# Kernel optimization log

Hardware: AMD Instinct MI355X
Metric: run time of the kernel (lower is better)

The kernel has to match this reference:

```python
import jax, jax.numpy as jnp
from jax import lax
import numpy as np

# Static config (see init_kwargs)
D_MODEL = 1024
K = 32          # num_heads
K_Q = 4         # num_query_heads
N_ANCHOR = 4
N_DECAY = K - N_ANCHOR  # 28
M = 8           # num_thetas
KS = 4          # conv kernel size
H = D_MODEL // K  # 32 (expand_factor=1 -> d_inner = d_model)
N_REP = K // K_Q  # 8
DIM_K = D_MODEL
DIM_DECAY = K
DIM_Q = K_Q * H * M * 2  # 2048
TOTAL = DIM_K + DIM_DECAY + DIM_Q  # 3104
B, L = 2, 2048


def setup_inputs() -> dict:
    key = jax.random.key(0)
    ks = jax.random.split(key, 8)
    x = jax.random.normal(ks[0], (B, L, D_MODEL), jnp.float32)
    W_in = jax.random.normal(ks[1], (D_MODEL, TOTAL), jnp.float32) * (D_MODEL ** -0.5)
    # depthwise causal conv kernel: (width, in_per_group=1, channels)
    conv_k = jax.random.normal(ks[2], (KS, 1, DIM_K + DIM_DECAY), jnp.float32) * 0.3
    # theta init (M > 1 branch): linspace(-pi/3, pi/3, M) tiled over (1,1,K,H,M)
    grid = np.linspace(-np.pi / 3, np.pi / 3, M)
    theta = jnp.asarray(np.tile(grid.reshape(1, 1, 1, 1, M), (1, 1, K, H, 1)), jnp.float32)
    decay_slopes = jnp.log(jnp.exp(jnp.asarray(np.geomspace(0.001, 0.1, N_DECAY), jnp.float32)) - 1.0)
    anchor_slopes = jnp.log(jnp.exp(jnp.asarray(np.geomspace(0.01, 0.1, N_ANCHOR), jnp.float32)) - 1.0)
    score_scale = jnp.ones((K,), jnp.float32)
    lim = float(np.sqrt(6.0 / (H + H)))  # glorot uniform
    W_re = jax.random.uniform(ks[3], (H, H), jnp.float32, -lim, lim)
    W_im = jax.random.uniform(ks[4], (H, H), jnp.float32, -lim, lim)
    norm_scale = jnp.ones((2 * H,), jnp.float32)
    W_out = jax.random.normal(ks[5], (D_MODEL, D_MODEL), jnp.float32) * (D_MODEL ** -0.5)
    return dict(x=x, W_in=W_in, conv_k=conv_k, theta=theta, decay_slopes=decay_slopes,
                anchor_slopes=anchor_slopes, score_scale=score_scale, W_re=W_re,
                W_im=W_im, norm_scale=norm_scale, W_out=W_out)


def reference(x, W_in, conv_k, theta, decay_slopes, anchor_slopes, score_scale,
              W_re, W_im, norm_scale, W_out):
    b, l, _ = x.shape
    z = x @ W_in                                    # (b,l,TOTAL)
    z_mem = z[..., :DIM_K + DIM_DECAY]
    q_raw = z[..., DIM_K + DIM_DECAY:]
    # causal depthwise conv over time
    zp = jnp.pad(z_mem, ((0, 0), (KS - 1, 0), (0, 0)))
    z_mem = lax.conv_general_dilated(zp, conv_k, window_strides=(1,), padding='VALID',
                                     dimension_numbers=('NWC', 'WIO', 'NWC'),
                                     feature_group_count=DIM_K + DIM_DECAY)
    k_val = z_mem[..., :DIM_K].reshape(b, l, K, H)
    s_raw = z_mem[..., -K:].reshape(b, l, K, 1)
    q = q_raw.reshape(b, l, K_Q, H, M, 2)
    q_re, q_im = q[..., 0], q[..., 1]
    # ALiBi-like decay / anchor log weights
    pos = jnp.arange(l, dtype=jnp.float32)
    slopes_d = jax.nn.softplus(decay_slopes).reshape(1, 1, N_DECAY, 1)
    dist = jnp.maximum(jnp.float32(l - 1) - pos, 0.0)
    lw_d = -slopes_d * dist[None, :, None, None]        # (1,l,N_DECAY,1)
    slopes_a = jax.nn.softplus(anchor_slopes).reshape(1, 1, N_ANCHOR, 1)
    lw_a = -slopes_a * pos[None, :, None, None]         # (1,l,N_ANCHOR,1)
    log_tw = jnp.concatenate([lw_d, lw_a], axis=2)      # (1,l,K,1)
    log_p = jnp.clip(score_scale[None, None, :, None] * s_raw, -20.0, 20.0)
    p_w = jnp.exp(log_p + log_tw)                       # (b,l,K,1)
    # complex rotary features of keys
    phi = k_val[..., None] * theta                      # (b,l,K,H,M)
    re_k = jnp.cos(phi)
    im_k = jnp.sin(phi)
    # cumulative state
    den = jnp.cumsum(p_w[..., 0], axis=1)               # (b,l,K)
    pwb = p_w[..., None]                                # (b,l,K,1,1)
    num_re = jnp.cumsum(pwb * re_k, axis=1)             # (b,l,K,H,M)
    num_im = jnp.cumsum(pwb * im_k, axis=1)
    inv = lax.rsqrt(jnp.maximum(den, 0.0001))
    inv = (inv * inv)[..., None, None]                  # 1/den, (b,l,K,1,1)
    s_re = (num_re * inv).reshape(b, l, K_Q, N_REP, H, M)
    s_im = (num_im * inv).reshape(b, l, K_Q, N_REP, H, M)
    qr = q_re.reshape(b, l, K_Q, 1, H, M)
    qi = q_im.reshape(b, l, K_Q, 1, H, M)
    out_re = jnp.sum(s_re * qr + s_im * qi, axis=-1).reshape(b, l, K, H)
    out_im = jnp.sum(s_im * qr - s_re * qi, axis=-1).reshape(b, l, K, H)
    # original einsum 'blkh,hh->blkh' uses only the diagonal of W_re / W_im
    y_re = out_re * norm_scale[:H] * jnp.diagonal(W_re)
    y_im = out_im * norm_scale[H:] * jnp.diagonal(W_im)
    y = jax.nn.silu((y_re + y_im).reshape(b, l, DIM_K))
    return y @ W_out
```

## Files before the change

kernel.cpp:

```cpp
#include <hip/hip_runtime.h>
#include <hip/hip_bf16.h>
#include <math.h>

#define D_MODEL   1024
#define K_TOT     32
#define N_DECAY   28
#define M_DIM     8
#define KS        4
#define H_DIM     32
#define DIM_K     1024
#define DIM_MEM   1056
#define DIM_Q     2048
#define TOTAL_DIM 3104
#define NPAD_IN   3328
#define B_SZ      2
#define L_SEQ     2048
#define BL_TOT    4096

#define KG_CNT    4
#define NCHUNK    64
#define CHUNK_L   32

typedef __attribute__((ext_vector_type(8))) __bf16 bf16x8;
typedef __attribute__((ext_vector_type(4))) __bf16 bf16x4;
typedef __attribute__((ext_vector_type(4))) float  f32x4;

__device__ __forceinline__ void gload_lds16(const void* g, void* l) {
    __builtin_amdgcn_global_load_lds(
        (const __attribute__((address_space(1))) void*)g,
        (__attribute__((address_space(3))) void*)l, 16, 0, 0);
}

__global__ __launch_bounds__(512, 2) void gemm_big(const __bf16* __restrict__ A,
                                                   const __bf16* __restrict__ Bt,
                                                   float* __restrict__ C,
                                                   __bf16* __restrict__ Cq,
                                                   int Kdim, int gx) {
    __shared__ __bf16 lds[2][2][256 * 64];

    const int tid  = threadIdx.x;
    const int w    = tid >> 6;
    const int lane = tid & 63;
    const int l15  = lane & 15;
    const int l16  = lane >> 4;
    const int wm   = w >> 2;
    const int wn   = w & 3;

    const int nwg = gridDim.x;
    int lin = blockIdx.x;
    lin = (lin & 7) * (nwg >> 3) + (lin >> 3);
    const int bx = lin % gx, by = lin / gx;
    const int r0 = by * 256, c0 = bx * 256;

    const int srl   = lane >> 3;
    const int sslot = lane & 7;

    f32x4 acc[8][4] = {};
    const int NT = Kdim / 64;

#define STG_A(T, BUF, J)                                                       \
    {                                                                          \
        const int r_  = (J) * 64 + w * 8 + srl;                                \
        const int so_ = sslot ^ (r_ & 7);                                      \
        gload_lds16(A + (size_t)(r0 + r_) * Kdim + (T) * 64 + so_ * 8,         \
                    &lds[BUF][0][((J) * 64 + w * 8) * 64]);                    \
    }
#define STG_B(T, BUF, J)                                                       \
    {                                                                          \
        const int r_  = (J) * 64 + w * 8 + srl;                                \
        const int so_ = sslot ^ (r_ & 7);                                      \
        gload_lds16(Bt + (size_t)(c0 + r_) * Kdim + (T) * 64 + so_ * 8,        \
                    &lds[BUF][1][((J) * 64 + w * 8) * 64]);                    \
    }

#define LOAD_A(AP, MIBASE)                                                     \
    _Pragma("unroll") for (int m2 = 0; m2 < 2; m2++)                           \
        _Pragma("unroll") for (int kk = 0; kk < 2; kk++) {                     \
            const int row_  = wm * 128 + ((MIBASE) + m2) * 16 + l15;           \
            const int slot_ = (kk * 4 + l16) ^ (row_ & 7);                     \
            AP[m2][kk] = *(const bf16x8*)&As_[row_ * 64 + slot_ * 8];          \
        }

#define PHASE(AP, MIBASE)                                                      \
    __builtin_amdgcn_s_barrier();                                              \
    asm volatile("s_waitcnt lgkmcnt(0)" ::: "memory");                         \
    __builtin_amdgcn_sched_barrier(0);                                         \
    __builtin_amdgcn_s_setprio(1);                                             \
    _Pragma("unroll") for (int kk = 0; kk < 2; kk++)                           \
        _Pragma("unroll") for (int m2 = 0; m2 < 2; m2++)                       \
            _Pragma("unroll") for (int ni = 0; ni < 4; ni++)                   \
                acc[(MIBASE) + m2][ni] =                                       \
                    __builtin_amdgcn_mfma_f32_16x16x32_bf16(                   \
                        AP[m2][kk], b[ni][kk], acc[(MIBASE) + m2][ni], 0,0,0); \
    __builtin_amdgcn_s_setprio(0);                                             \
    __builtin_amdgcn_sched_barrier(0);                                         \
    __builtin_amdgcn_s_barrier();

#pragma unroll
    for (int j = 0; j < 4; j++) { STG_A(0, 0, j); STG_B(0, 0, j); }
#pragma unroll
    for (int j = 0; j < 4; j++) { STG_A(1, 1, j); STG_B(1, 1, j); }
    __builtin_amdgcn_sched_barrier(0);
    asm volatile("s_waitcnt vmcnt(8)" ::: "memory");
    __builtin_amdgcn_s_barrier();
    __builtin_amdgcn_sched_barrier(0);

    for (int t = 0; t < NT; ++t) {
        const int cur = t & 1;
        const __bf16* As_ = &lds[cur][0][0];
        const __bf16* Bs_ = &lds[cur][1][0];
        const bool pf = (t + 2 < NT);
        const int tn = t + 2;

        bf16x8 b[4][2], ap[2][2];

#pragma unroll
        for (int ni = 0; ni < 4; ni++)
#pragma unroll
            for (int kk = 0; kk < 2; kk++) {
                const int col  = wn * 64 + ni * 16 + l15;
                const int slot = (kk * 4 + l16) ^ (col & 7);
                b[ni][kk] = *(const bf16x8*)&Bs_[col * 64 + slot * 8];
            }
        LOAD_A(ap, 0);
        PHASE(ap, 0);

        LOAD_A(ap, 2);
        if (pf) { STG_B(tn, cur, 0); STG_B(tn, cur, 1); }
        PHASE(ap, 2);

        LOAD_A(ap, 4);
        if (pf) { STG_B(tn, cur, 2); STG_B(tn, cur, 3);
                  STG_A(tn, cur, 0); STG_A(tn, cur, 2); }
        PHASE(ap, 4);

        LOAD_A(ap, 6);
        PHASE(ap, 6);

        if (pf) { STG_A(tn, cur, 1); STG_A(tn, cur, 3); }
        __builtin_amdgcn_sched_barrier(0);
        if (pf) asm volatile("s_waitcnt vmcnt(8)" ::: "memory");
        else    asm volatile("s_waitcnt vmcnt(0)" ::: "memory");
        __builtin_amdgcn_s_barrier();
        __builtin_amdgcn_sched_barrier(0);
    }
#undef STG_A
#undef STG_B
#undef LOAD_A
#undef PHASE

#pragma unroll
    for (int mi = 0; mi < 8; mi++) {
#pragma unroll
        for (int ni = 0; ni < 4; ni++) {
            const int col = c0 + wn * 64 + ni * 16 + l15;
            const int row = r0 + wm * 128 + mi * 16 + l16 * 4;
            if (col < DIM_MEM) {
#pragma unroll
                for (int q = 0; q < 4; q++)
                    C[(size_t)(row + q) * DIM_MEM + col] = acc[mi][ni][q];
            } else if (col < TOTAL_DIM) {
#pragma unroll
                for (int q = 0; q < 4; q++)
                    Cq[(size_t)(row + q) * DIM_Q + (col - DIM_MEM)] =
                        (__bf16)acc[mi][ni][q];
            }
        }
    }
}

__global__ __launch_bounds__(512, 2) void gemm_mid(const __bf16* __restrict__ A,
                                                   const __bf16* __restrict__ Bt,
                                                   float* __restrict__ C,
                                                   int Ndim, int Kdim, int gx) {
    __shared__ __bf16 lds[2][2][128 * 64];

    const int tid  = threadIdx.x;
    const int w    = tid >> 6;
    const int lane = tid & 63;
    const int l15  = lane & 15;
    const int l16  = lane >> 4;
    const int wm   = w >> 1;
    const int wn   = w & 1;

    const int nwg = gridDim.x;
    int lin = blockIdx.x;
    lin = (lin & 7) * (nwg >> 3) + (lin >> 3);
    const int bx = lin % gx, by = lin / gx;
    const int r0 = by * 128, c0 = bx * 128;

    const int srl   = lane >> 3;
    const int sslot = lane & 7;

    f32x4 acc[2][4] = {};
    const int NT = Kdim / 64;

#define STG4(T, BUF)                                                           \
    _Pragma("unroll") for (int j = 0; j < 2; j++) {                            \
        const int r_  = j * 64 + w * 8 + srl;                                  \
        const int so_ = sslot ^ (r_ & 7);                                      \
        gload_lds16(A + (size_t)(r0 + r_) * Kdim + (T) * 64 + so_ * 8,         \
                    &lds[BUF][0][(j * 64 + w * 8) * 64]);                      \
        gload_lds16(Bt + (size_t)(c0 + r_) * Kdim + (T) * 64 + so_ * 8,        \
                    &lds[BUF][1][(j * 64 + w * 8) * 64]);                      \
    }

    STG4(0, 0);
    STG4(1, 1);
    __builtin_amdgcn_sched_barrier(0);
    asm volatile("s_waitcnt vmcnt(4)" ::: "memory");
    __builtin_amdgcn_s_barrier();
    __builtin_amdgcn_sched_barrier(0);

    for (int t = 0; t < NT; ++t) {
        const int cur = t & 1;
        const __bf16* As_ = &lds[cur][0][0];
        const __bf16* Bs_ = &lds[cur][1][0];
        const bool pf = (t + 2 < NT);

        bf16x8 b[4][2], a[2][2];
#pragma unroll
        for (int ni = 0; ni < 4; ni++)
#pragma unroll
            for (int kk = 0; kk < 2; kk++) {
                const int col  = wn * 64 + ni * 16 + l15;
                const int slot = (kk * 4 + l16) ^ (col & 7);
                b[ni][kk] = *(const bf16x8*)&Bs_[col * 64 + slot * 8];
            }
#pragma unroll
        for (int mi = 0; mi < 2; mi++)
#pragma unroll
            for (int kk = 0; kk < 2; kk++) {
                const int row  = wm * 32 + mi * 16 + l15;
                const int slot = (kk * 4 + l16) ^ (row & 7);
                a[mi][kk] = *(const bf16x8*)&As_[row * 64 + slot * 8];
            }
        asm volatile("s_waitcnt lgkmcnt(0)" ::: "memory");
        __builtin_amdgcn_sched_barrier(0);
        __builtin_amdgcn_s_setprio(1);
#pragma unroll
        for (int kk = 0; kk < 2; kk++)
#pragma unroll
            for (int mi = 0; mi < 2; mi++)
#pragma unroll
                for (int ni = 0; ni < 4; ni++)
                    acc[mi][ni] = __builtin_amdgcn_mfma_f32_16x16x32_bf16(
                        a[mi][kk], b[ni][kk], acc[mi][ni], 0, 0, 0);
        __builtin_amdgcn_s_setprio(0);
        __builtin_amdgcn_sched_barrier(0);
        __builtin_amdgcn_s_barrier();
        if (pf) STG4(t + 2, cur);
        __builtin_amdgcn_sched_barrier(0);
        if (pf) asm volatile("s_waitcnt vmcnt(4)" ::: "memory");
        else    asm volatile("s_waitcnt vmcnt(0)" ::: "memory");
        __builtin_amdgcn_s_barrier();
        __builtin_amdgcn_sched_barrier(0);
    }
#undef STG4

#pragma unroll
    for (int mi = 0; mi < 2; mi++) {
#pragma unroll
        for (int ni = 0; ni < 4; ni++) {
            const int col = c0 + wn * 64 + ni * 16 + l15;
            const int row = r0 + wm * 32 + mi * 16 + l16 * 4;
#pragma unroll
            for (int q = 0; q < 4; q++)
                C[(size_t)(row + q) * Ndim + col] = acc[mi][ni][q];
        }
    }
}

__global__ __launch_bounds__(256) void cast_bf16(const float* __restrict__ in,
                                                 __bf16* __restrict__ out, int n4) {
    const int i = blockIdx.x * blockDim.x + threadIdx.x;
    if (i >= n4) return;
    const float4 v = ((const float4*)in)[i];
    bf16x4 o;
    o.x = (__bf16)v.x; o.y = (__bf16)v.y; o.z = (__bf16)v.z; o.w = (__bf16)v.w;
    ((bf16x4*)out)[i] = o;
}

__global__ __launch_bounds__(256) void transpose_cast(const float* __restrict__ W,
                                                      __bf16* __restrict__ Wt,
                                                      int Kdim, int Ndim, int Npad) {
    __shared__ float tile[32][33];
    const int n0 = blockIdx.x * 32, k0 = blockIdx.y * 32;
    const int tx = threadIdx.x & 31, ty = threadIdx.x >> 5;
#pragma unroll
    for (int i = 0; i < 32; i += 8) {
        float v = 0.f;
        if (n0 + tx < Ndim) v = W[(size_t)(k0 + ty + i) * Ndim + n0 + tx];
        tile[ty + i][tx] = v;
    }
    __syncthreads();
#pragma unroll
    for (int i = 0; i < 32; i += 8) {
        const int n = n0 + ty + i;
        if (n < Npad) Wt[(size_t)n * Kdim + k0 + tx] = (__bf16)tile[tx][ty + i];
    }
}

__global__ __launch_bounds__(256) void conv_pw(const float* __restrict__ z_mem,
                                               const float* __restrict__ conv_k,
                                               const float* __restrict__ score_scale,
                                               const float* __restrict__ decay_slopes,
                                               const float* __restrict__ anchor_slopes,
                                               __bf16* __restrict__ k_val,
                                               float* __restrict__ p_w) {
    const int bl = blockIdx.x;
    const int l = bl & (L_SEQ - 1);
    const int b = bl >> 11;
    const int t = threadIdx.x;

    {
        const int c = 4 * t;
        float4 acc = {0.f, 0.f, 0.f, 0.f};
#pragma unroll
        for (int s = 0; s < KS; s++) {
            const int tl = l - (KS - 1) + s;
            if (tl >= 0) {
                const float4 ck = *(const float4*)&conv_k[s * DIM_MEM + c];
                const float4 zv = *(const float4*)&z_mem[((size_t)b * L_SEQ + tl) * DIM_MEM + c];
                acc.x = fmaf(ck.x, zv.x, acc.x);
                acc.y = fmaf(ck.y, zv.y, acc.y);
                acc.z = fmaf(ck.z, zv.z, acc.z);
                acc.w = fmaf(ck.w, zv.w, acc.w);
            }
        }
        bf16x4 o;
        o.x = (__bf16)acc.x; o.y = (__bf16)acc.y;
        o.z = (__bf16)acc.z; o.w = (__bf16)acc.w;
        *(bf16x4*)&k_val[(size_t)bl * DIM_K + c] = o;
    }

    if (t < 8) {
        const int c = DIM_MEM - K_TOT + 4 * t;
        float acc[4] = {0.f, 0.f, 0.f, 0.f};
#pragma unroll
        for (int s = 0; s < KS; s++) {
            const int tl = l - (KS - 1) + s;
            if (tl >= 0) {
                const float4 ck = *(const float4*)&conv_k[s * DIM_MEM + c];
                const float4 zv = *(const float4*)&z_mem[((size_t)b * L_SEQ + tl) * DIM_MEM + c];
                acc[0] = fmaf(ck.x, zv.x, acc[0]);
                acc[1] = fmaf(ck.y, zv.y, acc[1]);
                acc[2] = fmaf(ck.z, zv.z, acc[2]);
                acc[3] = fmaf(ck.w, zv.w, acc[3]);
            }
        }
#pragma unroll
        for (int j = 0; j < 4; j++) {
            const int k = 4 * t + j;
            const float lp = fminf(fmaxf(score_scale[k] * acc[j], -20.f), 20.f);
            float lt;
            if (k < N_DECAY) {
                const float sd = log1pf(__expf(decay_slopes[k]));
                lt = -sd * (float)(L_SEQ - 1 - l);
            } else {
                const float sa = log1pf(__expf(anchor_slopes[k - N_DECAY]));
                lt = -sa * (float)l;
            }
            p_w[(size_t)bl * K_TOT + k] = __expf(lp + lt);
        }
    }
}

__global__ __launch_bounds__(256) void chunk_sums(const __bf16* __restrict__ k_val,
                                                  const float* __restrict__ p_w,
                                                  const float* __restrict__ theta,
                                                  float* __restrict__ csum,
                                                  float* __restrict__ cden) {
    const int idx = blockIdx.x;
    const int c = idx & (NCHUNK - 1);
    const int bkg = idx / NCHUNK;
    const int kg = bkg & (KG_CNT - 1);
    const int b = bkg / KG_CNT;
    const int t = threadIdx.x;
    const int kl = t >> 5;
    const int h = t & 31;
    const int k = kg * 8 + kl;
    const int bk = b * K_TOT + k;

    const float A0 = theta[(k * H_DIM + h) * M_DIM + 0];
    const float Dt = theta[(k * H_DIM + h) * M_DIM + 1] - A0;

    float nre[M_DIM] = {}, nim[M_DIM] = {};
    float den = 0.f;
    const int l0 = c * CHUNK_L;
#pragma unroll 2
    for (int i = 0; i < CHUNK_L; i++) {
        const size_t bl = (size_t)b * L_SEQ + (l0 + i);
        const float p  = p_w[bl * K_TOT + k];
        const float kv = (float)k_val[bl * DIM_K + k * H_DIM + h];
        float cc = __cosf(kv * A0), ss = __sinf(kv * A0);
        const float cd = __cosf(kv * Dt), sd = __sinf(kv * Dt);
#pragma unroll
        for (int m = 0; m < M_DIM; m++) {
            nre[m] = fmaf(p, cc, nre[m]);
            nim[m] = fmaf(p, ss, nim[m]);
            const float c2 = fmaf(cc, cd, -(ss * sd));
            ss = fmaf(ss, cd, cc * sd);
            cc = c2;
        }
        den += p;
    }

    float* base = &csum[(((size_t)bk * NCHUNK + c) * 256 + h * M_DIM) * 2];
#pragma unroll
    for (int j = 0; j < 4; j++) {
        f32x4 v = { nre[2 * j], nim[2 * j], nre[2 * j + 1], nim[2 * j + 1] };
        ((f32x4*)base)[j] = v;
    }
    if (h == 0) cden[bk * NCHUNK + c] = den;
}

__global__ __launch_bounds__(256) void chunk_prefix(float* __restrict__ csum,
                                                    float* __restrict__ cden) {
    const int bk = blockIdx.x;
    const int t = threadIdx.x;

    if (t < 64) {
        const float orig = cden[bk * NCHUNK + t];
        float v = orig;
#pragma unroll
        for (int d = 1; d < 64; d <<= 1) {
            const float u = __shfl_up(v, d);
            if (t >= d) v += u;
        }
        cden[bk * NCHUNK + t] = v - orig;
    }

    float run_re = 0.f, run_im = 0.f;
    for (int c = 0; c < NCHUNK; c++) {
        float2* p = (float2*)&csum[(((size_t)bk * NCHUNK + c) * 256 + t) * 2];
        const float2 v = *p;
        *p = make_float2(run_re, run_im);
        run_re += v.x;
        run_im += v.y;
    }
}

__global__ __launch_bounds__(256) void scan_out(const __bf16* __restrict__ q_b,
                                                const __bf16* __restrict__ k_val,
                                                const float* __restrict__ p_w,
                                                const float* __restrict__ theta,
                                                const float* __restrict__ csum,
                                                const float* __restrict__ cden,
                                                const float* __restrict__ W_re,
                                                const float* __restrict__ W_im,
                                                const float* __restrict__ norm_scale,
                                                __bf16* __restrict__ y) {
    const int idx = blockIdx.x;
    const int c = idx & (NCHUNK - 1);
    const int bkg = idx / NCHUNK;
    const int kg = bkg & (KG_CNT - 1);
    const int b = bkg / KG_CNT;
    const int t = threadIdx.x;
    const int kl = t >> 5;
    const int h = t & 31;
    const int k = kg * 8 + kl;
    const int bk = b * K_TOT + k;

    const float A0 = theta[(k * H_DIM + h) * M_DIM + 0];
    const float Dt = theta[(k * H_DIM + h) * M_DIM + 1] - A0;

    float nre[M_DIM], nim[M_DIM];
    {
        const float* base = &csum[(((size_t)bk * NCHUNK + c) * 256 + h * M_DIM) * 2];
#pragma unroll
        for (int j = 0; j < 4; j++) {
            const f32x4 v = ((const f32x4*)base)[j];
            nre[2 * j] = v.x; nim[2 * j] = v.y;
            nre[2 * j + 1] = v.z; nim[2 * j + 1] = v.w;
        }
    }
    float den = cden[bk * NCHUNK + c];

    const float wsc_re = norm_scale[h] * W_re[h * H_DIM + h];
    const float wsc_im = norm_scale[H_DIM + h] * W_im[h * H_DIM + h];

    const int l0 = c * CHUNK_L;
    for (int i = 0; i < CHUNK_L; i++) {
        const size_t bl = (size_t)b * L_SEQ + (l0 + i);
        const float p  = p_w[bl * K_TOT + k];
        const float kv = (float)k_val[bl * DIM_K + k * H_DIM + h];

        const __bf16* qp = &q_b[bl * DIM_Q + (size_t)(kg * H_DIM + h) * 16];
        const bf16x8 q0 = *(const bf16x8*)qp;
        const bf16x8 q1 = *(const bf16x8*)(qp + 8);

        float cc = __cosf(kv * A0), ss = __sinf(kv * A0);
        const float cd = __cosf(kv * Dt), sd = __sinf(kv * Dt);

        float ore = 0.f, oim = 0.f;
#pragma unroll
        for (int m = 0; m < M_DIM; m++) {
            nre[m] = fmaf(p, cc, nre[m]);
            nim[m] = fmaf(p, ss, nim[m]);
            const float qr = (m < 4) ? (float)q0[2 * (m & 3)]     : (float)q1[2 * (m & 3)];
            const float qi = (m < 4) ? (float)q0[2 * (m & 3) + 1] : (float)q1[2 * (m & 3) + 1];
            ore = fmaf(nre[m], qr, fmaf(nim[m], qi, ore));
            oim = fmaf(nim[m], qr, fmaf(-nre[m], qi, oim));
            const float c2 = fmaf(cc, cd, -(ss * sd));
            ss = fmaf(ss, cd, cc * sd);
            cc = c2;
        }
        den += p;
        const float inv = __builtin_amdgcn_rcpf(fmaxf(den, 1e-4f));

        const float v = (ore * wsc_re + oim * wsc_im) * inv;
        const float yv = v * __builtin_amdgcn_rcpf(1.0f + __expf(-v));
        y[bl * DIM_K + k * H_DIM + h] = (__bf16)yv;
    }
}

extern "C" void kernel_launch(void* const* d_in, const int* in_sizes, int n_in,
                              void* d_out, int out_size, void* d_ws, size_t ws_size,
                              hipStream_t stream) {
    const float* x            = (const float*)d_in[0];
    const float* W_in         = (const float*)d_in[1];
    const float* conv_k       = (const float*)d_in[2];
    const float* theta        = (const float*)d_in[3];
    const float* decay_slopes = (const float*)d_in[4];
    const float* anchor_slopes= (const float*)d_in[5];
    const float* score_scale  = (const float*)d_in[6];
    const float* W_re         = (const float*)d_in[7];
    const float* W_im         = (const float*)d_in[8];
    const float* norm_scale   = (const float*)d_in[9];
    const float* W_out        = (const float*)d_in[10];
    float* out = (float*)d_out;

    float* ws = (float*)d_ws;
    size_t off = 0;
    float* z_mem  = ws + off; off += (size_t)BL_TOT * DIM_MEM;
    float* p_w    = ws + off; off += (size_t)BL_TOT * K_TOT;
    float* csum   = ws + off; off += (size_t)B_SZ * K_TOT * NCHUNK * 256 * 2;
    float* cden   = ws + off; off += (size_t)B_SZ * K_TOT * NCHUNK;
    __bf16* k_val   = (__bf16*)(ws + off); off += (size_t)BL_TOT * DIM_K / 2;
    __bf16* x_b     = (__bf16*)(ws + off); off += (size_t)BL_TOT * D_MODEL / 2;
    __bf16* W_in_T  = (__bf16*)(ws + off); off += (size_t)NPAD_IN * D_MODEL / 2;
    __bf16* W_out_T = (__bf16*)(ws + off); off += (size_t)D_MODEL * D_MODEL / 2;
    __bf16* y_b     = (__bf16*)(ws + off); off += (size_t)BL_TOT * DIM_K / 2;
    __bf16* q_b     = (__bf16*)(ws + off); off += (size_t)BL_TOT * DIM_Q / 2;

    cast_bf16<<<(BL_TOT * D_MODEL / 4 + 255) / 256, 256, 0, stream>>>(
        x, x_b, BL_TOT * D_MODEL / 4);
    {
        dim3 g(NPAD_IN / 32, D_MODEL / 32);
        transpose_cast<<<g, 256, 0, stream>>>(W_in, W_in_T, D_MODEL, TOTAL_DIM, NPAD_IN);
    }
    {
        dim3 g(D_MODEL / 32, D_MODEL / 32);
        transpose_cast<<<g, 256, 0, stream>>>(W_out, W_out_T, D_MODEL, D_MODEL, D_MODEL);
    }

    gemm_big<<<(NPAD_IN / 256) * (BL_TOT / 256), 512, 0, stream>>>(
        x_b, W_in_T, z_mem, q_b, D_MODEL, NPAD_IN / 256);

    conv_pw<<<BL_TOT, 256, 0, stream>>>(z_mem, conv_k, score_scale, decay_slopes,
                                        anchor_slopes, k_val, p_w);
    chunk_sums<<<B_SZ * KG_CNT * NCHUNK, 256, 0, stream>>>(k_val, p_w, theta, csum, cden);
    chunk_prefix<<<B_SZ * K_TOT, 256, 0, stream>>>(csum, cden);
    scan_out<<<B_SZ * KG_CNT * NCHUNK, 256, 0, stream>>>(q_b, k_val, p_w, theta, csum,
                                                         cden, W_re, W_im, norm_scale, y_b);
    gemm_mid<<<(D_MODEL / 128) * (BL_TOT / 128), 512, 0, stream>>>(
        y_b, W_out_T, out, D_MODEL, D_MODEL, D_MODEL / 128);
}
```

Before: 125.8 us.

## Fuse causal conv and p_w computation into chunk_sums and scan_out

```diff
diff --git a/kernel.cpp b/kernel.cpp
--- a/kernel.cpp
+++ b/kernel.cpp
@@ -301,73 +301,45 @@
     }
 }
 
-__global__ __launch_bounds__(256) void conv_pw(const float* __restrict__ z_mem,
-                                               const float* __restrict__ conv_k,
-                                               const float* __restrict__ score_scale,
-                                               const float* __restrict__ decay_slopes,
-                                               const float* __restrict__ anchor_slopes,
-                                               __bf16* __restrict__ k_val,
-                                               float* __restrict__ p_w) {
-    const int bl = blockIdx.x;
-    const int l = bl & (L_SEQ - 1);
-    const int b = bl >> 11;
-    const int t = threadIdx.x;
-
-    {
-        const int c = 4 * t;
-        float4 acc = {0.f, 0.f, 0.f, 0.f};
-#pragma unroll
-        for (int s = 0; s < KS; s++) {
-            const int tl = l - (KS - 1) + s;
-            if (tl >= 0) {
-                const float4 ck = *(const float4*)&conv_k[s * DIM_MEM + c];
-                const float4 zv = *(const float4*)&z_mem[((size_t)b * L_SEQ + tl) * DIM_MEM + c];
-                acc.x = fmaf(ck.x, zv.x, acc.x);
-                acc.y = fmaf(ck.y, zv.y, acc.y);
-                acc.z = fmaf(ck.z, zv.z, acc.z);
-                acc.w = fmaf(ck.w, zv.w, acc.w);
-            }
-        }
-        bf16x4 o;
-        o.x = (__bf16)acc.x; o.y = (__bf16)acc.y;
-        o.z = (__bf16)acc.z; o.w = (__bf16)acc.w;
-        *(bf16x4*)&k_val[(size_t)bl * DIM_K + c] = o;
-    }
-
-    if (t < 8) {
-        const int c = DIM_MEM - K_TOT + 4 * t;
-        float acc[4] = {0.f, 0.f, 0.f, 0.f};
-#pragma unroll
-        for (int s = 0; s < KS; s++) {
-            const int tl = l - (KS - 1) + s;
-            if (tl >= 0) {
-                const float4 ck = *(const float4*)&conv_k[s * DIM_MEM + c];
-                const float4 zv = *(const float4*)&z_mem[((size_t)b * L_SEQ + tl) * DIM_MEM + c];
-                acc[0] = fmaf(ck.x, zv.x, acc[0]);
-                acc[1] = fmaf(ck.y, zv.y, acc[1]);
-                acc[2] = fmaf(ck.z, zv.z, acc[2]);
-                acc[3] = fmaf(ck.w, zv.w, acc[3]);
-            }
-        }
-#pragma unroll
-        for (int j = 0; j < 4; j++) {
-            const int k = 4 * t + j;
-            const float lp = fminf(fmaxf(score_scale[k] * acc[j], -20.f), 20.f);
-            float lt;
-            if (k < N_DECAY) {
-                const float sd = log1pf(__expf(decay_slopes[k]));
-                lt = -sd * (float)(L_SEQ - 1 - l);
-            } else {
-                const float sa = log1pf(__expf(anchor_slopes[k - N_DECAY]));
-                lt = -sa * (float)l;
-            }
-            p_w[(size_t)bl * K_TOT + k] = __expf(lp + lt);
-        }
-    }
-}
-
-__global__ __launch_bounds__(256) void chunk_sums(const __bf16* __restrict__ k_val,
-                                                  const float* __restrict__ p_w,
+struct ConvCtx {
+    float ck0, ck1, ck2, ck3;
+    float gk0, gk1, gk2, gk3;
+    float ssc, c0_, c1_;
+    int   ch, gc;
+};
+
+__device__ __forceinline__ ConvCtx make_ctx(const float* __restrict__ conv_k,
+                                            const float* __restrict__ score_scale,
+                                            const float* __restrict__ decay_slopes,
+                                            const float* __restrict__ anchor_slopes,
+                                            int k, int h) {
+    ConvCtx cx;
+    cx.ch = k * H_DIM + h;
+    cx.gc = DIM_K + k;
+    cx.ck0 = conv_k[0 * DIM_MEM + cx.ch];
+    cx.ck1 = conv_k[1 * DIM_MEM + cx.ch];
+    cx.ck2 = conv_k[2 * DIM_MEM + cx.ch];
+    cx.ck3 = conv_k[3 * DIM_MEM + cx.ch];
+    cx.gk0 = conv_k[0 * DIM_MEM + cx.gc];
+    cx.gk1 = conv_k[1 * DIM_MEM + cx.gc];
+    cx.gk2 = conv_k[2 * DIM_MEM + cx.gc];
+    cx.gk3 = conv_k[3 * DIM_MEM + cx.gc];
+    cx.ssc = score_scale[k];
+    if (k < N_DECAY) {
+        const float sd = log1pf(__expf(decay_slopes[k]));
+        cx.c0_ = -sd * (float)(L_SEQ - 1); cx.c1_ = sd;
+    } else {
+        const float sa = log1pf(__expf(anchor_slopes[k - N_DECAY]));
+        cx.c0_ = 0.f; cx.c1_ = -sa;
+    }
+    return cx;
+}
+
+__global__ __launch_bounds__(256) void chunk_sums(const float* __restrict__ z_mem,
+                                                  const float* __restrict__ conv_k,
+                                                  const float* __restrict__ score_scale,
+                                                  const float* __restrict__ decay_slopes,
+                                                  const float* __restrict__ anchor_slopes,
                                                   const float* __restrict__ theta,
                                                   float* __restrict__ csum,
                                                   float* __restrict__ cden) {
@@ -382,17 +354,35 @@
     const int k = kg * 8 + kl;
     const int bk = b * K_TOT + k;
 
+    const ConvCtx cx = make_ctx(conv_k, score_scale, decay_slopes, anchor_slopes, k, h);
+
     const float A0 = theta[(k * H_DIM + h) * M_DIM + 0];
     const float Dt = theta[(k * H_DIM + h) * M_DIM + 1] - A0;
 
+    const int l0 = c * CHUNK_L;
+    const float* zb = z_mem + (size_t)b * L_SEQ * DIM_MEM;
+
+    float z1 = (l0 >= 3) ? zb[(size_t)(l0 - 3) * DIM_MEM + cx.ch] : 0.f;
+    float z2 = (l0 >= 2) ? zb[(size_t)(l0 - 2) * DIM_MEM + cx.ch] : 0.f;
+    float z3 = (l0 >= 1) ? zb[(size_t)(l0 - 1) * DIM_MEM + cx.ch] : 0.f;
+    float g1 = (l0 >= 3) ? zb[(size_t)(l0 - 3) * DIM_MEM + cx.gc] : 0.f;
+    float g2 = (l0 >= 2) ? zb[(size_t)(l0 - 2) * DIM_MEM + cx.gc] : 0.f;
+    float g3 = (l0 >= 1) ? zb[(size_t)(l0 - 1) * DIM_MEM + cx.gc] : 0.f;
+
     float nre[M_DIM] = {}, nim[M_DIM] = {};
     float den = 0.f;
-    const int l0 = c * CHUNK_L;
 #pragma unroll 2
     for (int i = 0; i < CHUNK_L; i++) {
-        const size_t bl = (size_t)b * L_SEQ + (l0 + i);
-        const float p  = p_w[bl * K_TOT + k];
-        const float kv = (float)k_val[bl * DIM_K + k * H_DIM + h];
+        const int l = l0 + i;
+        const float z0 = zb[(size_t)l * DIM_MEM + cx.ch];
+        const float g0 = zb[(size_t)l * DIM_MEM + cx.gc];
+        const float kv = fmaf(cx.ck0, z1, fmaf(cx.ck1, z2, fmaf(cx.ck2, z3, cx.ck3 * z0)));
+        const float gv = fmaf(cx.gk0, g1, fmaf(cx.gk1, g2, fmaf(cx.gk2, g3, cx.gk3 * g0)));
+        z1 = z2; z2 = z3; z3 = z0;
+        g1 = g2; g2 = g3; g3 = g0;
+        const float lp = fminf(fmaxf(cx.ssc * gv, -20.f), 20.f);
+        const float p  = __expf(lp + cx.c0_ + cx.c1_ * (float)l);
+
         float cc = __cosf(kv * A0), ss = __sinf(kv * A0);
         const float cd = __cosf(kv * Dt), sd = __sinf(kv * Dt);
 #pragma unroll
@@ -441,9 +431,12 @@
     }
 }
 
-__global__ __launch_bounds__(256) void scan_out(const __bf16* __restrict__ q_b,
-                                                const __bf16* __restrict__ k_val,
-                                                const float* __restrict__ p_w,
+__global__ __launch_bounds__(256) void scan_out(const float* __restrict__ z_mem,
+                                                const __bf16* __restrict__ q_b,
+                                                const float* __restrict__ conv_k,
+                                                const float* __restrict__ score_scale,
+                                                const float* __restrict__ decay_slopes,
+                                                const float* __restrict__ anchor_slopes,
                                                 const float* __restrict__ theta,
                                                 const float* __restrict__ csum,
                                                 const float* __restrict__ cden,
@@ -462,6 +455,8 @@
     const int k = kg * 8 + kl;
     const int bk = b * K_TOT + k;
 
+    const ConvCtx cx = make_ctx(conv_k, score_scale, decay_slopes, anchor_slopes, k, h);
+
     const float A0 = theta[(k * H_DIM + h) * M_DIM + 0];
     const float Dt = theta[(k * H_DIM + h) * M_DIM + 1] - A0;
 
@@ -481,10 +476,26 @@
     const float wsc_im = norm_scale[H_DIM + h] * W_im[h * H_DIM + h];
 
     const int l0 = c * CHUNK_L;
+    const float* zb = z_mem + (size_t)b * L_SEQ * DIM_MEM;
+
+    float z1 = (l0 >= 3) ? zb[(size_t)(l0 - 3) * DIM_MEM + cx.ch] : 0.f;
+    float z2 = (l0 >= 2) ? zb[(size_t)(l0 - 2) * DIM_MEM + cx.ch] : 0.f;
+    float z3 = (l0 >= 1) ? zb[(size_t)(l0 - 1) * DIM_MEM + cx.ch] : 0.f;
+    float g1 = (l0 >= 3) ? zb[(size_t)(l0 - 3) * DIM_MEM + cx.gc] : 0.f;
+    float g2 = (l0 >= 2) ? zb[(size_t)(l0 - 2) * DIM_MEM + cx.gc] : 0.f;
+    float g3 = (l0 >= 1) ? zb[(size_t)(l0 - 1) * DIM_MEM + cx.gc] : 0.f;
+
     for (int i = 0; i < CHUNK_L; i++) {
-        const size_t bl = (size_t)b * L_SEQ + (l0 + i);
-        const float p  = p_w[bl * K_TOT + k];
-        const float kv = (float)k_val[bl * DIM_K + k * H_DIM + h];
+        const int l = l0 + i;
+        const size_t bl = (size_t)b * L_SEQ + l;
+        const float z0 = zb[(size_t)l * DIM_MEM + cx.ch];
+        const float g0 = zb[(size_t)l * DIM_MEM + cx.gc];
+        const float kv = fmaf(cx.ck0, z1, fmaf(cx.ck1, z2, fmaf(cx.ck2, z3, cx.ck3 * z0)));
+        const float gv = fmaf(cx.gk0, g1, fmaf(cx.gk1, g2, fmaf(cx.gk2, g3, cx.gk3 * g0)));
+        z1 = z2; z2 = z3; z3 = z0;
+        g1 = g2; g2 = g3; g3 = g0;
+        const float lp = fminf(fmaxf(cx.ssc * gv, -20.f), 20.f);
+        const float p  = __expf(lp + cx.c0_ + cx.c1_ * (float)l);
 
         const __bf16* qp = &q_b[bl * DIM_Q + (size_t)(kg * H_DIM + h) * 16];
         const bf16x8 q0 = *(const bf16x8*)qp;
@@ -534,10 +545,8 @@
     float* ws = (float*)d_ws;
     size_t off = 0;
     float* z_mem  = ws + off; off += (size_t)BL_TOT * DIM_MEM;
-    float* p_w    = ws + off; off += (size_t)BL_TOT * K_TOT;
     float* csum   = ws + off; off += (size_t)B_SZ * K_TOT * NCHUNK * 256 * 2;
     float* cden   = ws + off; off += (size_t)B_SZ * K_TOT * NCHUNK;
-    __bf16* k_val   = (__bf16*)(ws + off); off += (size_t)BL_TOT * DIM_K / 2;
     __bf16* x_b     = (__bf16*)(ws + off); off += (size_t)BL_TOT * D_MODEL / 2;
     __bf16* W_in_T  = (__bf16*)(ws + off); off += (size_t)NPAD_IN * D_MODEL / 2;
     __bf16* W_out_T = (__bf16*)(ws + off); off += (size_t)D_MODEL * D_MODEL / 2;
@@ -558,12 +567,13 @@
     gemm_big<<<(NPAD_IN / 256) * (BL_TOT / 256), 512, 0, stream>>>(
         x_b, W_in_T, z_mem, q_b, D_MODEL, NPAD_IN / 256);
 
-    conv_pw<<<BL_TOT, 256, 0, stream>>>(z_mem, conv_k, score_scale, decay_slopes,
-                                        anchor_slopes, k_val, p_w);
-    chunk_sums<<<B_SZ * KG_CNT * NCHUNK, 256, 0, stream>>>(k_val, p_w, theta, csum, cden);
+    chunk_sums<<<B_SZ * KG_CNT * NCHUNK, 256, 0, stream>>>(
+        z_mem, conv_k, score_scale, decay_slopes, anchor_slopes, theta, csum, cden);
     chunk_prefix<<<B_SZ * K_TOT, 256, 0, stream>>>(csum, cden);
-    scan_out<<<B_SZ * KG_CNT * NCHUNK, 256, 0, stream>>>(q_b, k_val, p_w, theta, csum,
-                                                         cden, W_re, W_im, norm_scale, y_b);
+    scan_out<<<B_SZ * KG_CNT * NCHUNK, 256, 0, stream>>>(
+        z_mem, q_b, conv_k, score_scale, decay_slopes, anchor_slopes, theta,
+        csum, cden, W_re, W_im, norm_scale, y_b);
+
     gemm_mid<<<(D_MODEL / 128) * (BL_TOT / 128), 512, 0, stream>>>(
         y_b, W_out_T, out, D_MODEL, D_MODEL, D_MODEL / 128);
 }
```

Result: slower. 134.2 us (+6.6%).
